# Performance work log

Hardware: AMD Instinct MI355X
Metric: run time of the kernel (lower is better)

## Reference

```python
import jax, jax.numpy as jnp
import numpy as np

N, E, EL = 50000, 150000, 300000   # atoms, bonds(=line-graph nodes), line-graph edges
FN, FE, FX = 128, 128, 64          # atom, bond, angle feature dims (encode_dim)
H, D = 4, 64                        # num_heads, per-head hidden
SLOPE = 0.01                        # torch leaky_relu default


def _leaky(x):
    return jnp.where(x >= 0, x, SLOPE * x)


def _seg_softmax(logits, seg, n):
    # softmax over edges grouped by destination (DGL edge_softmax). logits [E, H]
    m = jax.ops.segment_max(logits, seg, num_segments=n)
    ex = jnp.exp(logits - m[seg])
    s = jax.ops.segment_sum(ex, seg, num_segments=n)
    return ex / s[seg]


def _seg_mean(x, seg, n):
    # mean of incoming edge feats per dst node; empty segments -> 0 (DGL behavior)
    s = jax.ops.segment_sum(x, seg, num_segments=n)
    c = jax.ops.segment_sum(jnp.ones((x.shape[0], 1), x.dtype), seg, num_segments=n)
    return s / jnp.maximum(c, 1.0)


def setup_inputs() -> dict:
    key = jax.random.key(0)
    ks = iter(jax.random.split(key, 40))
    nrm = lambda shape, sc=0.1: jax.random.normal(next(ks), shape, jnp.float32) * sc
    z = lambda n: jnp.zeros((n,), jnp.float32)
    inp = {
        'nfeats': nrm((N, FN), 1.0),
        'efeats': nrm((E, FE), 1.0),
        'xfeats': nrm((EL, FX), 1.0),
        # EGAT layer (atom graph)
        'e_Wni': nrm((H * D, FN)), 'e_Wnj': nrm((H * D, FN)), 'e_Wfij': nrm((H * D, FE)),
        'e_Wnode': nrm((H * D, FN + FE)), 'e_bnode': z(H * D),
        'e_attn': nrm((H, D)), 'e_bias': z(H * D),
        # Path_Complex line-graph branch
        'lg_Wni': nrm((H * D, D)), 'lg_Wnj': nrm((H * D, D)), 'lg_Wfij': nrm((H * D, FX)),
        'lg_Wnode': nrm((H * D, D + FX)), 'lg_bnode': z(H * D),
        'lg_attn': nrm((H, D)), 'lg_bias': z(H * D),
        # Path_Complex graph branch
        'g_Wni': nrm((H * D, D)), 'g_Wnj': nrm((H * D, D)), 'g_Wfij': nrm((H * D, D)),
        'g_Wnode': nrm((H * D, D + D)), 'g_bnode': z(H * D),
        'g_attn': nrm((H, D)), 'g_bias': z(H * D),
        # graph / line-graph connectivity
        'src': jax.random.randint(next(ks), (E,), 0, N, jnp.int32),
        'dst': jax.random.randint(next(ks), (E,), 0, N, jnp.int32),
        'lsrc': jax.random.randint(next(ks), (EL,), 0, E, jnp.int32),
        'ldst': jax.random.randint(next(ks), (EL,), 0, E, jnp.int32),
    }
    return inp


def _forward(nfeats, efeats, xfeats,
             e_Wni, e_Wnj, e_Wfij, e_Wnode, e_bnode, e_attn, e_bias,
             lg_Wni, lg_Wnj, lg_Wfij, lg_Wnode, lg_bnode, lg_attn, lg_bias,
             g_Wni, g_Wnj, g_Wfij, g_Wnode, g_bnode, g_attn, g_bias,
             src, dst, lsrc, ldst):
    # ---- EGAT layer on atom graph ----
    fo = _leaky((nfeats @ e_Wni.T)[src] + (nfeats @ e_Wnj.T)[dst] + efeats @ e_Wfij.T + e_bias)
    fov = fo.reshape(E, H, D)
    e_att = _seg_softmax((fov * e_attn[None]).sum(-1), dst, N)      # [E, H]
    agg = _seg_mean(efeats, dst, N)                                   # [N, FE]
    h = (jnp.concatenate([nfeats, agg], 1) @ e_Wnode.T + e_bnode).reshape(N, H, D)
    h_node = _leaky(jax.ops.segment_sum(h[src] * e_att[:, :, None], dst, num_segments=N)).sum(1)
    f_edge = fov.sum(1)                                               # [E, D]

    # ---- Path_Complex layer: line-graph (bond->angle) branch ----
    lgf = _leaky((f_edge @ lg_Wni.T)[lsrc] + (f_edge @ lg_Wnj.T)[ldst] + xfeats @ lg_Wfij.T + lg_bias)
    lgv = lgf.reshape(EL, H, D)
    a_lg = _seg_softmax((lgv * lg_attn[None]).sum(-1), ldst, E)      # [EL, H]
    aggx = _seg_mean(xfeats, ldst, E)                                 # [E, FX]
    m1 = (jnp.concatenate([f_edge, aggx], 1) @ lg_Wnode.T + lg_bnode).reshape(E, H, D)
    lg_h = _leaky(jax.ops.segment_sum(m1[lsrc] * a_lg[:, :, None], ldst, num_segments=E)).sum(1)

    # ---- Path_Complex layer: graph (atom->bond) branch ----
    gf = _leaky((h_node @ g_Wni.T)[src] + (h_node @ g_Wnj.T)[dst] + f_edge @ g_Wfij.T + g_bias)
    gv = gf.reshape(E, H, D)
    a_g = _seg_softmax((gv * g_attn[None]).sum(-1), dst, N)          # [E, H] -> l_graph ndata 'a'
    node_edge = h_node[src] + h_node[dst]
    m2 = (jnp.concatenate([node_edge, f_edge], 1) @ g_Wnode.T + g_bnode).reshape(E, H, D)
    # u_mul_v on line graph: message = h_out[lsrc] * a[ldst]
    g_h = _leaky(jax.ops.segment_sum(m2[lsrc] * a_g[ldst][:, :, None], ldst, num_segments=E)).sum(1)

    return g_h + lg_h                                                 # [E, D] updated bond feats


def reference(nfeats, efeats, xfeats,
              e_Wni, e_Wnj, e_Wfij, e_Wnode, e_bnode, e_attn, e_bias,
              lg_Wni, lg_Wnj, lg_Wfij, lg_Wnode, lg_bnode, lg_attn, lg_bias,
              g_Wni, g_Wnj, g_Wfij, g_Wnode, g_bnode, g_attn, g_bias,
              src, dst, lsrc, ldst):
    return _forward(nfeats, efeats, xfeats,
                    e_Wni, e_Wnj, e_Wfij, e_Wnode, e_bnode, e_attn, e_bias,
                    lg_Wni, lg_Wnj, lg_Wfij, lg_Wnode, lg_bnode, lg_attn, lg_bias,
                    g_Wni, g_Wnj, g_Wfij, g_Wnode, g_bnode, g_attn, g_bias,
                    src, dst, lsrc, ldst)
```

## Files before the change

### kernel.cpp

```cpp
#include <hip/hip_runtime.h>
#include <hip/hip_bf16.h>
#include <math.h>

typedef __hip_bfloat16 bf16;
typedef short bf16x8 __attribute__((ext_vector_type(8)));
typedef short s16x4 __attribute__((ext_vector_type(4)));
typedef float f32x4 __attribute__((ext_vector_type(4)));

__device__ __forceinline__ float b2f(bf16 x) { return __bfloat162float(x); }
__device__ __forceinline__ bf16  f2b(float x) { return __float2bfloat16(x); }
__device__ __forceinline__ float leaky(float x) { return x >= 0.0f ? x : 0.01f * x; }
__device__ __forceinline__ float sb2f(short s) {
  return __uint_as_float(((unsigned)(unsigned short)s) << 16);
}
__device__ __forceinline__ short f2bs(float x) {
  unsigned u = __float_as_uint(x);
  u += 0x7FFFu + ((u >> 16) & 1u);
  return (short)(u >> 16);
}
__device__ __forceinline__ float ldF(const void* p, size_t i, int f) {
  return f ? ((const float*)p)[i] : b2f(((const bf16*)p)[i]);
}
__device__ __forceinline__ bf16x8 ldA8(const char* row, int k, int f) {
  if (!f) return *(const bf16x8*)(row + (size_t)k * 2);
  const float4* p = (const float4*)(row + (size_t)k * 4);
  float4 a = p[0], b = p[1];
  bf16x8 r;
  r[0] = f2bs(a.x); r[1] = f2bs(a.y); r[2] = f2bs(a.z); r[3] = f2bs(a.w);
  r[4] = f2bs(b.x); r[5] = f2bs(b.y); r[6] = f2bs(b.z); r[7] = f2bs(b.w);
  return r;
}

__global__ void k_detect(const unsigned* __restrict__ w, int* __restrict__ flag) {
  __shared__ int cnt[256];
  unsigned x = w[threadIdx.x];
  unsigned ex = (x >> 7) & 0xFFu;
  cnt[threadIdx.x] = (ex >= 96u && ex <= 144u) ? 1 : 0;
  __syncthreads();
  for (int s = 128; s > 0; s >>= 1) {
    if (threadIdx.x < s) cnt[threadIdx.x] += cnt[threadIdx.x + s];
    __syncthreads();
  }
  if (threadIdx.x == 0) *flag = (cnt[0] < 128) ? 1 : 0;
}

struct WArgs { const void* src[21]; int beg[22]; int len[21]; };
__global__ void k_cvt_all(WArgs wa, bf16* __restrict__ dst, int total,
                          const int* __restrict__ flagp) {
  int f = *flagp;
  for (int i = blockIdx.x * 256 + threadIdx.x; i < total; i += gridDim.x * 256) {
    int t = 0;
    while (t < 20 && i >= wa.beg[t + 1]) ++t;
    int loc = i - wa.beg[t];
    bf16 v = f2b(0.0f);
    if (loc < wa.len[t])
      v = f ? f2b(((const float*)wa.src[t])[loc]) : ((const bf16*)wa.src[t])[loc];
    dst[i] = v;
  }
}

__global__ void k_cvt2(const float* __restrict__ a, bf16* __restrict__ da, size_t na,
                       const float* __restrict__ c, bf16* __restrict__ dc, size_t nc,
                       const int* __restrict__ flagp) {
  if (!*flagp) return;
  size_t tot = (na + nc) >> 2;
  for (size_t i = (size_t)blockIdx.x * 256 + threadIdx.x; i < tot;
       i += (size_t)gridDim.x * 256) {
    size_t j = i << 2;
    const float* s; bf16* d; size_t loc;
    if (j < na) { s = a; d = da; loc = j; }
    else        { s = c; d = dc; loc = j - na; }
    float4 v = *(const float4*)(s + loc);
    s16x4 o; o[0] = f2bs(v.x); o[1] = f2bs(v.y); o[2] = f2bs(v.z); o[3] = f2bs(v.w);
    *(s16x4*)(d + loc) = o;
  }
}

__global__ void k_cvt1(const float* __restrict__ c, bf16* __restrict__ dc, size_t nc,
                       const int* __restrict__ flagp) {
  if (!*flagp) return;
  size_t tot = nc >> 2;
  for (size_t i = (size_t)blockIdx.x * 256 + threadIdx.x; i < tot;
       i += (size_t)gridDim.x * 256) {
    size_t loc = i << 2;
    float4 v = *(const float4*)(c + loc);
    s16x4 o; o[0] = f2bs(v.x); o[1] = f2bs(v.y); o[2] = f2bs(v.z); o[3] = f2bs(v.w);
    *(s16x4*)(dc + loc) = o;
  }
}

__global__ void k_izero(int* __restrict__ p, int n) {
  int i = blockIdx.x * 256 + threadIdx.x;
  for (; i < n; i += gridDim.x * 256) p[i] = 0;
}

__global__ void k_hist(const int* __restrict__ seg, int* __restrict__ deg, int n) {
  int i = blockIdx.x * 256 + threadIdx.x;
  if (i < n) atomicAdd(&deg[seg[i]], 1);
}

__global__ __launch_bounds__(256)
void k_scan_local(const int* __restrict__ deg, int* __restrict__ rp,
                  int* __restrict__ bsum, int n) {
  __shared__ int sh[256];
  int tid = threadIdx.x;
  int base = blockIdx.x * 4096 + tid * 16;
  int v[16]; int s = 0;
#pragma unroll
  for (int j = 0; j < 16; ++j) { v[j] = (base + j < n) ? deg[base + j] : 0; s += v[j]; }
  sh[tid] = s;
  __syncthreads();
  for (int o = 1; o < 256; o <<= 1) {
    int t = (tid >= o) ? sh[tid - o] : 0;
    __syncthreads();
    sh[tid] += t;
    __syncthreads();
  }
  int run = sh[tid] - s;
#pragma unroll
  for (int j = 0; j < 16; ++j) {
    run += v[j];
    if (base + j < n) rp[base + j + 1] = run;
  }
  if (tid == 255) bsum[blockIdx.x] = sh[255];
  if (blockIdx.x == 0 && tid == 0) rp[0] = 0;
}
__global__ __launch_bounds__(256)
void k_scan_bsum(int* __restrict__ bsum, int nb) {
  __shared__ int sh[256];
  __shared__ int carry;
  int tid = threadIdx.x;
  if (tid == 0) carry = 0;
  __syncthreads();
  for (int base = 0; base < nb; base += 256) {
    int i = base + tid;
    int v = (i < nb) ? bsum[i] : 0;
    sh[tid] = v;
    __syncthreads();
    for (int o = 1; o < 256; o <<= 1) {
      int t = (tid >= o) ? sh[tid - o] : 0;
      __syncthreads();
      sh[tid] += t;
      __syncthreads();
    }
    if (i < nb) bsum[i] = carry + sh[tid] - v;
    int tot = sh[255];
    __syncthreads();
    if (tid == 0) carry += tot;
    __syncthreads();
  }
}
__global__ __launch_bounds__(256)
void k_scan_add(int* __restrict__ rp, const int* __restrict__ bsum, int n) {
  int b = blockIdx.x + 1;
  int ofs = bsum[b];
  int base = b * 4096 + threadIdx.x * 16;
#pragma unroll
  for (int j = 0; j < 16; ++j) {
    int idx = base + j + 1;
    if (idx <= n) rp[idx] += ofs;
  }
}

__global__ void k_slot(const int* __restrict__ seg, const int* __restrict__ rp,
                       int* __restrict__ cur, int* __restrict__ eid,
                       const int* __restrict__ aux1, int* __restrict__ av1,
                       int* __restrict__ pos, int n) {
  int i = blockIdx.x * 256 + threadIdx.x;
  if (i >= n) return;
  int t = seg[i];
  int p = atomicAdd(&cur[t], 1);
  int j = rp[t] + p;
  eid[j] = i;
  if (av1) av1[j] = aux1[i];
  if (pos) pos[i] = j;
}

__global__ void k_gmean(const void* __restrict__ X, const void* __restrict__ Xc, int mode,
                        const int* __restrict__ rp, const int* __restrict__ eid,
                        bf16* __restrict__ out, int n, int width,
                        const int* __restrict__ flagp) {
  int f = (mode == 2) ? *flagp : mode;
  if (Xc && f) { X = Xc; f = 0; }
  int d = threadIdx.x;
  int row = blockIdx.x * blockDim.y + threadIdx.y;
  if (row >= n) return;
  int b = rp[row], e = rp[row + 1];
  float s = 0.0f;
  for (int j = b; j < e; ++j) s += ldF(X, (size_t)eid[j] * width + d, f);
  out[(size_t)row * width + d] = f2b(s / fmaxf((float)(e - b), 1.0f));
}

__global__ __launch_bounds__(256)
void k_mgemm(const void* __restrict__ A0, const void* __restrict__ A0c, int m0mode, int K0,
             const void* __restrict__ A1, int m1mode, int Ktot,
             const bf16* __restrict__ W, int whs, const bf16* __restrict__ bias,
             bf16* __restrict__ C, int cs, int M,
             const int* __restrict__ flagp) {
  int tid = threadIdx.x;
  int w = tid >> 6, lane = tid & 63, l15 = lane & 15, q = lane >> 4;
  int h = blockIdx.y;
  int fl = *flagp;
  int f0 = (m0mode == 2) ? fl : m0mode;
  if (A0c && f0) { A0 = A0c; f0 = 0; }
  int f1 = (m1mode == 2) ? fl : m1mode;
  const bf16* Wh = W + (size_t)h * whs;
  int colofs = h * 64;
  int m0 = blockIdx.x * 64 + w * 16;
  int mA = m0 + l15; if (mA > M - 1) mA = M - 1;
  const char* rowA0 = (const char*)A0 + (size_t)mA * K0 * (f0 ? 4 : 2);
  const char* rowA1 = A1 ? (const char*)A1 + (size_t)mA * (Ktot - K0) * (f1 ? 4 : 2) : nullptr;

  f32x4 acc[4] = {{0,0,0,0},{0,0,0,0},{0,0,0,0},{0,0,0,0}};
  for (int k = q * 8; k < Ktot; k += 32) {
    bf16x8 a;
    if (k < K0) a = ldA8(rowA0, k, f0);
    else        a = ldA8(rowA1, k - K0, f1);
    const bf16* wb = Wh + (size_t)l15 * Ktot + k;
#pragma unroll
    for (int t = 0; t < 4; ++t)
      acc[t] = __builtin_amdgcn_mfma_f32_16x16x32_bf16(
          a, *(const bf16x8*)(wb + (size_t)(t * 16) * Ktot), acc[t], 0, 0, 0);
  }
#pragma unroll
  for (int t = 0; t < 4; ++t) {
    int col = t * 16 + l15;
    float bv = bias ? b2f(bias[colofs + col]) : 0.0f;
#pragma unroll
    for (int r = 0; r < 4; ++r) {
      int m = m0 + q * 4 + r;
      if (m < M) C[(size_t)m * cs + colofs + col] = f2b(acc[t][r] + bv);
    }
  }
}

__global__ __launch_bounds__(256)
void k_mgemm2sw(const void* __restrict__ A, const void* __restrict__ Ac, int mode, int K,
                const bf16* __restrict__ W1, const bf16* __restrict__ W2, int whs,
                int h0, int HB, bf16* __restrict__ C1, bf16* __restrict__ C2, int M,
                const int* __restrict__ flagp) {
  int tid = threadIdx.x;
  int w = tid >> 6, lane = tid & 63, l15 = lane & 15, q = lane >> 4;
  int hy = blockIdx.y;
  int h = h0 + hy;
  int f = (mode == 2) ? *flagp : mode;
  if (Ac && f) { A = Ac; f = 0; }
  const bf16* W1h = W1 + (size_t)h * whs;
  const bf16* W2h = W2 + (size_t)h * whs;
  int cs = HB * 64;
  int m0 = blockIdx.x * 64 + w * 16;
  int mA = m0 + l15; if (mA > M - 1) mA = M - 1;
  const char* rowA = (const char*)A + (size_t)mA * K * (f ? 4 : 2);

  f32x4 a1[4] = {{0,0,0,0},{0,0,0,0},{0,0,0,0},{0,0,0,0}};
  f32x4 a2[4] = {{0,0,0,0},{0,0,0,0},{0,0,0,0},{0,0,0,0}};
  for (int k = q * 8; k < K; k += 32) {
    bf16x8 a = ldA8(rowA, k, f);
    const bf16* w1 = W1h + (size_t)l15 * K + k;
    const bf16* w2 = W2h + (size_t)l15 * K + k;
#pragma unroll
    for (int t = 0; t < 4; ++t) {
      a1[t] = __builtin_amdgcn_mfma_f32_16x16x32_bf16(
          a, *(const bf16x8*)(w1 + (size_t)(t * 16) * K), a1[t], 0, 0, 0);
      a2[t] = __builtin_amdgcn_mfma_f32_16x16x32_bf16(
          a, *(const bf16x8*)(w2 + (size_t)(t * 16) * K), a2[t], 0, 0, 0);
    }
  }
  int ofs = l15 * 4 * HB + hy * 4;
#pragma unroll
  for (int r = 0; r < 4; ++r) {
    int m = m0 + q * 4 + r;
    if (m < M) {
      s16x4 o1, o2;
#pragma unroll
      for (int t = 0; t < 4; ++t) { o1[t] = f2bs(a1[t][r]); o2[t] = f2bs(a2[t][r]); }
      *(s16x4*)(C1 + (size_t)m * cs + ofs) = o1;
      *(s16x4*)(C2 + (size_t)m * cs + ofs) = o2;
    }
  }
}

template<int NK>
__global__ __launch_bounds__(256)
void k_mcomb4sw(const bf16* __restrict__ A, const bf16* __restrict__ Ac,
                const bf16* __restrict__ W, int whs,
                const bf16* __restrict__ bias, const bf16* __restrict__ attn,
                const bf16* __restrict__ G1, const bf16* __restrict__ G2,
                const int* __restrict__ gi, const int* __restrict__ gj,
                const int* __restrict__ posw,
                float* __restrict__ lg4, bf16* __restrict__ fout,
                int M, const int* __restrict__ flagp) {
  constexpr int K = NK * 32;
  int tid = threadIdx.x;
  int w = tid >> 6, lane = tid & 63, l15 = lane & 15, q = lane >> 4;
  if (Ac && *flagp) A = Ac;
  int m0 = blockIdx.x * 64 + w * 16;
  int mA = m0 + l15; if (mA > M - 1) mA = M - 1;
  const bf16* rowA = A + (size_t)mA * K;
  bf16x8 af[NK];
#pragma unroll
  for (int i = 0; i < NK; ++i) af[i] = *(const bf16x8*)(rowA + q * 8 + 32 * i);
  int pIdx[4]; bool okr[4];
  bf16x8 gv1[4][2], gv2[4][2];
#pragma unroll
  for (int r = 0; r < 4; ++r) {
    int m = m0 + q * 4 + r;
    okr[r] = m < M; int mc = okr[r] ? m : M - 1;
    pIdx[r] = posw ? posw[mc] : mc;
    const bf16* p1 = G1 + (size_t)gi[mc] * 256 + l15 * 16;
    const bf16* p2 = G2 + (size_t)gj[mc] * 256 + l15 * 16;
    gv1[r][0] = *(const bf16x8*)p1; gv1[r][1] = *(const bf16x8*)(p1 + 8);
    gv2[r][0] = *(const bf16x8*)p2; gv2[r][1] = *(const bf16x8*)(p2 + 8);
  }
  f32x4 fs[4] = {{0,0,0,0},{0,0,0,0},{0,0,0,0},{0,0,0,0}};
#pragma unroll
  for (int h = 0; h < 4; ++h) {
    const bf16* Wh = W + (size_t)h * whs;
    f32x4 acc[4] = {{0,0,0,0},{0,0,0,0},{0,0,0,0},{0,0,0,0}};
#pragma unroll
    for (int i = 0; i < NK; ++i) {
      const bf16* wb = Wh + (size_t)l15 * K + q * 8 + 32 * i;
#pragma unroll
      for (int t = 0; t < 4; ++t)
        acc[t] = __builtin_amdgcn_mfma_f32_16x16x32_bf16(
            af[i], *(const bf16x8*)(wb + (size_t)(t * 16) * K), acc[t], 0, 0, 0);
    }
    float bv[4], av[4];
#pragma unroll
    for (int t = 0; t < 4; ++t) {
      bv[t] = b2f(bias[h * 64 + t * 16 + l15]);
      av[t] = b2f(attn[h * 64 + t * 16 + l15]);
    }
    float part[4];
#pragma unroll
    for (int r = 0; r < 4; ++r) {
      float p = 0.0f;
#pragma unroll
      for (int t = 0; t < 4; ++t) {
        float v = acc[t][r] + bv[t] + sb2f(gv1[r][h >> 1][(h & 1) * 4 + t])
                                    + sb2f(gv2[r][h >> 1][(h & 1) * 4 + t]);
        v = leaky(v);
        p += v * av[t];
        fs[t][r] += v;
      }
      part[r] = p;
    }
#pragma unroll
    for (int o = 1; o < 16; o <<= 1)
#pragma unroll
      for (int r = 0; r < 4; ++r) part[r] += __shfl_xor(part[r], o, 64);
    if (l15 == 0) {
#pragma unroll
      for (int r = 0; r < 4; ++r)
        if (okr[r]) lg4[(size_t)pIdx[r] * 4 + h] = part[r];
    }
  }
  if (fout) {
#pragma unroll
    for (int t = 0; t < 4; ++t) {
      int col = t * 16 + l15;
#pragma unroll
      for (int r = 0; r < 4; ++r)
        if (okr[r]) fout[(size_t)(m0 + q * 4 + r) * 64 + col] = f2b(fs[t][r]);
    }
  }
}

template<int NK>
__global__ __launch_bounds__(256)
void k_mcomb2h(const bf16* __restrict__ A, const bf16* __restrict__ Ac,
               const bf16* __restrict__ W, int whs, int h0,
               const bf16* __restrict__ bias, const bf16* __restrict__ attn,
               const bf16* __restrict__ G1, const bf16* __restrict__ G2,
               const int* __restrict__ gi, const int* __restrict__ gj,
               const int* __restrict__ posw,
               float* __restrict__ lg4, int M, const int* __restrict__ flagp) {
  constexpr int K = NK * 32;
  int tid = threadIdx.x;
  int w = tid >> 6, lane = tid & 63, l15 = lane & 15, q = lane >> 4;
  if (Ac && *flagp) A = Ac;
  int m0 = blockIdx.x * 64 + w * 16;
  int mA = m0 + l15; if (mA > M - 1) mA = M - 1;
  const bf16* rowA = A + (size_t)mA * K;
  bf16x8 af[NK];
#pragma unroll
  for (int i = 0; i < NK; ++i) af[i] = *(const bf16x8*)(rowA + q * 8 + 32 * i);
  int pIdx[4]; bool okr[4];
  bf16x8 gv1[4], gv2[4];
#pragma unroll
  for (int r = 0; r < 4; ++r) {
    int m = m0 + q * 4 + r;
    okr[r] = m < M; int mc = okr[r] ? m : M - 1;
    pIdx[r] = posw ? posw[mc] : mc;
    gv1[r] = *(const bf16x8*)(G1 + (size_t)gi[mc] * 128 + l15 * 8);
    gv2[r] = *(const bf16x8*)(G2 + (size_t)gj[mc] * 128 + l15 * 8);
  }
#pragma unroll
  for (int hy = 0; hy < 2; ++hy) {
    int h = h0 + hy;
    const bf16* Wh = W + (size_t)h * whs;
    f32x4 acc[4] = {{0,0,0,0},{0,0,0,0},{0,0,0,0},{0,0,0,0}};
#pragma unroll
    for (int i = 0; i < NK; ++i) {
      const bf16* wb = Wh + (size_t)l15 * K + q * 8 + 32 * i;
#pragma unroll
      for (int t = 0; t < 4; ++t)
        acc[t] = __builtin_amdgcn_mfma_f32_16x16x32_bf16(
            af[i], *(const bf16x8*)(wb + (size_t)(t * 16) * K), acc[t], 0, 0, 0);
    }
    float bv[4], av[4];
#pragma unroll
    for (int t = 0; t < 4; ++t) {
      bv[t] = b2f(bias[h * 64 + t * 16 + l15]);
      av[t] = b2f(attn[h * 64 + t * 16 + l15]);
    }
    float part[4];
#pragma unroll
    for (int r = 0; r < 4; ++r) {
      float p = 0.0f;
#pragma unroll
      for (int t = 0; t < 4; ++t) {
        float v = acc[t][r] + bv[t] + sb2f(gv1[r][hy * 4 + t]) + sb2f(gv2[r][hy * 4 + t]);
        p += leaky(v) * av[t];
      }
      part[r] = p;
    }
#pragma unroll
    for (int o = 1; o < 16; o <<= 1)
#pragma unroll
      for (int r = 0; r < 4; ++r) part[r] += __shfl_xor(part[r], o, 64);
    if (l15 == 0) {
#pragma unroll
      for (int r = 0; r < 4; ++r)
        if (okr[r]) lg4[(size_t)pIdx[r] * 4 + h] = part[r];
    }
  }
}

__global__ __launch_bounds__(256)
void k_smax4_csr(float* __restrict__ lg, const int* __restrict__ rp, int n) {
  int tid = blockIdx.x * 256 + threadIdx.x;
  int row = tid >> 2, h = tid & 3;
  if (row >= n) return;
  int b = rp[row], e = rp[row + 1];
  float m = -INFINITY;
  for (int j = b; j < e; ++j) m = fmaxf(m, lg[(size_t)j * 4 + h]);
  float s = 0.0f;
  for (int j = b; j < e; ++j) {
    float ex = expf(lg[(size_t)j * 4 + h] - m);
    lg[(size_t)j * 4 + h] = ex;
    s += ex;
  }
  float inv = 1.0f / s;
  for (int j = b; j < e; ++j) lg[(size_t)j * 4 + h] *= inv;
}
__global__ __launch_bounds__(256)
void k_smax4_eid(float* __restrict__ lg, const int* __restrict__ rp,
                 const int* __restrict__ eid, int n) {
  int tid = blockIdx.x * 256 + threadIdx.x;
  int row = tid >> 2, h = tid & 3;
  if (row >= n) return;
  int b = rp[row], e = rp[row + 1];
  float m = -INFINITY;
  for (int j = b; j < e; ++j) m = fmaxf(m, lg[(size_t)eid[j] * 4 + h]);
  float s = 0.0f;
  for (int j = b; j < e; ++j) {
    float ex = expf(lg[(size_t)eid[j] * 4 + h] - m);
    lg[(size_t)eid[j] * 4 + h] = ex;
    s += ex;
  }
  float inv = 1.0f / s;
  for (int j = b; j < e; ++j) lg[(size_t)eid[j] * 4 + h] *= inv;
}

__global__ __launch_bounds__(256)
void k_ghnode(const bf16* __restrict__ H, const float* __restrict__ lg4c,
              const int* __restrict__ rp, const int* __restrict__ srcv,
              bf16* __restrict__ hnode, int N) {
  int d = threadIdx.x, h = threadIdx.y;
  int n = blockIdx.x;
  int b = rp[n], e = rp[n + 1];
  float s = 0.0f;
  for (int j = b; j < e; ++j)
    s += b2f(H[(size_t)srcv[j] * 256 + h * 64 + d]) * lg4c[(size_t)j * 4 + h];
  float v = leaky(s);
  __shared__ float sh[4][64];
  if (h > 0) sh[h][d] = v;
  __syncthreads();
  if (h == 0)
    hnode[(size_t)n * 64 + d] = f2b(v + sh[1][d] + sh[2][d] + sh[3][d]);
}

__global__ void k_gout2(const bf16* __restrict__ M1, const float* __restrict__ lgE4,
                        int h, const int* __restrict__ rp, const int* __restrict__ lsv,
                        float* __restrict__ out, int E, int first) {
  int d = threadIdx.x;
  int t = blockIdx.x * 4 + threadIdx.y;
  if (t >= E) return;
  int b = rp[t], e = rp[t + 1];
  float s = 0.0f;
  for (int j = b; j < e; ++j)
    s += b2f(M1[(size_t)lsv[j] * 64 + d]) * lgE4[(size_t)j * 4 + h];
  float val = leaky(s);
  if (first) out[(size_t)t * 64 + d] = val;
  else       out[(size_t)t * 64 + d] += val;
}

__global__ void k_gagg(const bf16* __restrict__ ne, const bf16* __restrict__ fe,
                       const int* __restrict__ rp, const int* __restrict__ lsv,
                       bf16* __restrict__ agg, int E) {
  int d = threadIdx.x;
  int t = blockIdx.x * 4 + threadIdx.y;
  if (t >= E) return;
  int b = rp[t], e = rp[t + 1];
  float s1 = 0.0f, s2 = 0.0f;
  for (int j = b; j < e; ++j) {
    size_t row = (size_t)lsv[j] * 64 + d;
    s1 += b2f(ne[row]);
    s2 += b2f(fe[row]);
  }
  agg[(size_t)t * 128 + d]      = f2b(s1);
  agg[(size_t)t * 128 + 64 + d] = f2b(s2);
}

__global__ __launch_bounds__(256)
void k_mgemm3(const bf16* __restrict__ A, const bf16* __restrict__ W, int whs,
              const bf16* __restrict__ bias, const float* __restrict__ lg4n,
              const int* __restrict__ rp, float* __restrict__ out, int M) {
  int tid = threadIdx.x;
  int w = tid >> 6, lane = tid & 63, l15 = lane & 15, q = lane >> 4;
  int m0 = blockIdx.x * 64 + w * 16;
  int mA = m0 + l15; if (mA > M - 1) mA = M - 1;
  const bf16* rowA = A + (size_t)mA * 128;
  bf16x8 af[4];
#pragma unroll
  for (int i = 0; i < 4; ++i) af[i] = *(const bf16x8*)(rowA + q * 8 + 32 * i);
  bool okr[4]; float degv[4]; float av[4][4];
#pragma unroll
  for (int r = 0; r < 4; ++r) {
    int m = m0 + q * 4 + r;
    okr[r] = m < M; int mc = okr[r] ? m : M - 1;
    degv[r] = (float)(rp[mc + 1] - rp[mc]);
#pragma unroll
    for (int h = 0; h < 4; ++h) av[r][h] = lg4n[(size_t)mc * 4 + h];
  }
  float osum[4][4] = {{0,0,0,0},{0,0,0,0},{0,0,0,0},{0,0,0,0}};
#pragma unroll
  for (int h = 0; h < 4; ++h) {
    const bf16* Wh = W + (size_t)h * whs;
    f32x4 acc[4] = {{0,0,0,0},{0,0,0,0},{0,0,0,0},{0,0,0,0}};
#pragma unroll
    for (int i = 0; i < 4; ++i) {
      const bf16* wb = Wh + (size_t)l15 * 128 + q * 8 + 32 * i;
#pragma unroll
      for (int t = 0; t < 4; ++t)
        acc[t] = __builtin_amdgcn_mfma_f32_16x16x32_bf16(
            af[i], *(const bf16x8*)(wb + (size_t)(t * 16) * 128), acc[t], 0, 0, 0);
    }
#pragma unroll
    for (int t = 0; t < 4; ++t) {
      float bv = b2f(bias[h * 64 + t * 16 + l15]);
#pragma unroll
      for (int r = 0; r < 4; ++r)
        osum[t][r] += leaky(av[r][h] * (acc[t][r] + degv[r] * bv));
    }
  }
#pragma unroll
  for (int t = 0; t < 4; ++t) {
    int col = t * 16 + l15;
#pragma unroll
    for (int r = 0; r < 4; ++r) {
      int m = m0 + q * 4 + r;
      if (m < M) out[(size_t)m * 64 + col] += osum[t][r];
    }
  }
}

__global__ void k_addpair(const bf16* __restrict__ hn, const int* __restrict__ src,
                          const int* __restrict__ dst, bf16* __restrict__ ne, int E) {
  int d = threadIdx.x;
  int e = blockIdx.x * 4 + threadIdx.y;
  if (e >= E) return;
  ne[(size_t)e * 64 + d] =
      f2b(b2f(hn[(size_t)src[e] * 64 + d]) + b2f(hn[(size_t)dst[e] * 64 + d]));
}

__global__ void k_cast(void* __restrict__ out, const float* __restrict__ a, size_t n,
                       const int* __restrict__ flagp) {
  int f = *flagp;
  size_t i = (size_t)blockIdx.x * blockDim.x + threadIdx.x;
  size_t st = (size_t)gridDim.x * blockDim.x;
  for (; i < n; i += st) {
    if (f) ((float*)out)[i] = a[i];
    else   ((bf16*)out)[i] = f2b(a[i]);
  }
}

extern "C" void kernel_launch(void* const* d_in, const int* in_sizes, int n_in,
                              void* d_out, int out_size, void* d_ws, size_t ws_size,
                              hipStream_t stream) {
  const int* src  = (const int*)d_in[24];
  const int* dst  = (const int*)d_in[25];
  const int* lsrc = (const int*)d_in[26];
  const int* ldst = (const int*)d_in[27];

  const int N  = in_sizes[0] / 128;
  const int E  = in_sizes[24];
  const int EL = in_sizes[26];
  (void)n_in; (void)out_size; (void)ws_size;

  char* base = (char*)d_ws;
  size_t off = 0;
  auto alloc = [&](size_t bytes) -> char* {
    char* p = base + off;
    off = (off + bytes + 255) & ~(size_t)255;
    return p;
  };
  int* flag = (int*)alloc(256);
  size_t wofs[28]; size_t wtot = 0;
  for (int i = 3; i <= 23; ++i) { wofs[i] = wtot; wtot += (size_t)((in_sizes[i] + 127) & ~127); }
  bf16* WA = (bf16*)alloc(wtot * 2);

  int*   tmpi  = (int*)alloc((size_t)2 * E * 4);
  int*   rpN   = (int*)alloc((size_t)(N + 1) * 4);
  int*   eidN  = (int*)alloc((size_t)E * 4);
  int*   srcv  = (int*)alloc((size_t)E * 4);
  int*   posN  = (int*)alloc((size_t)E * 4);
  int*   rpE   = (int*)alloc((size_t)(E + 1) * 4);
  int*   eidEL = (int*)alloc((size_t)EL * 4);
  int*   lsv   = (int*)alloc((size_t)EL * 4);
  int*   posE  = (int*)alloc((size_t)EL * 4);
  int*   bsum  = (int*)alloc(((size_t)((E > N ? E : N) + 4095) / 4096 + 8) * 4);
  bf16*  fedge = (bf16*)alloc((size_t)E * 64 * 2);
  bf16*  hnode = (bf16*)alloc((size_t)N * 64 * 2);
  float* outacc= (float*)alloc((size_t)E * 64 * 4);
  bf16*  aggB  = (bf16*)alloc((size_t)E * 64 * 2);
  size_t saElems = (size_t)E * 128 > (size_t)N * 256 ? (size_t)E * 128 : (size_t)N * 256;
  bf16*  SA    = (bf16*)alloc(saElems * 2);
  float* logE4 = (float*)alloc((size_t)E * 4 * 4);
  float* logEL4= (float*)alloc((size_t)EL * 4 * 4);
  bf16*  nb    = (bf16*)alloc((size_t)N * 128 * 2);

  bf16* SBo = (bf16*)outacc;
  bf16* eb = (bf16*)d_out;
  bf16* xb = (bf16*)d_out;

  dim3 blk(256);
  const unsigned tN = (N + 63) / 64, tEg = (E + 63) / 64, tELg = (EL + 63) / 64;
  const unsigned gE4 = (E + 3) / 4;
  const unsigned cE = (E + 255) / 256, cEL = (EL + 255) / 256;
  const int nbN = (N + 4095) / 4096, nbE = (E + 4095) / 4096;

  k_detect<<<dim3(1), blk, 0, stream>>>((const unsigned*)d_in[0], flag);
  WArgs wa;
  for (int i = 3; i <= 23; ++i) {
    wa.src[i - 3] = d_in[i];
    wa.beg[i - 3] = (int)wofs[i];
    wa.len[i - 3] = in_sizes[i];
  }
  wa.beg[21] = (int)wtot;
  k_cvt_all<<<dim3(512), blk, 0, stream>>>(wa, WA, (int)wtot, flag);
  k_cvt2<<<dim3(2048), blk, 0, stream>>>(
      (const float*)d_in[0], nb, (size_t)N * 128,
      (const float*)d_in[1], eb, (size_t)E * 128, flag);

  int* deg = tmpi; int* cur = tmpi + E;
  k_izero<<<dim3(1024), blk, 0, stream>>>(tmpi, 2 * E);
  k_hist<<<dim3(cE), blk, 0, stream>>>(dst, deg, E);
  k_scan_local<<<dim3(nbN), blk, 0, stream>>>(deg, rpN, bsum, N);
  k_scan_bsum<<<dim3(1), blk, 0, stream>>>(bsum, nbN);
  if (nbN > 1) k_scan_add<<<dim3(nbN - 1), blk, 0, stream>>>(rpN, bsum, N);
  k_slot<<<dim3(cE), blk, 0, stream>>>(dst, rpN, cur, eidN, src, srcv, posN, E);
  k_izero<<<dim3(1024), blk, 0, stream>>>(tmpi, 2 * E);
  k_hist<<<dim3(cEL), blk, 0, stream>>>(ldst, deg, EL);
  k_scan_local<<<dim3(nbE), blk, 0, stream>>>(deg, rpE, bsum, E);
  k_scan_bsum<<<dim3(1), blk, 0, stream>>>(bsum, nbE);
  if (nbE > 1) k_scan_add<<<dim3(nbE - 1), blk, 0, stream>>>(rpE, bsum, E);
  k_slot<<<dim3(cEL), blk, 0, stream>>>(ldst, rpE, cur, eidEL, lsrc, lsv, posE, EL);

  k_gmean<<<dim3((N + 1) / 2), dim3(128, 2), 0, stream>>>(d_in[1], eb, 2, rpN, eidN,
                                                          aggB, N, 128, flag);
  k_mgemm2sw<<<dim3(tN, 4), blk, 0, stream>>>(d_in[0], nb, 2, 128,
      WA + wofs[3], WA + wofs[4], 8192, 0, 4, SA, SBo, N, flag);
  k_mcomb4sw<4><<<dim3(tEg), blk, 0, stream>>>((const bf16*)d_in[1], eb,
      WA + wofs[5], 8192, WA + wofs[9], WA + wofs[8], SA, SBo,
      src, dst, posN, logE4, fedge, E, flag);
  k_smax4_csr<<<dim3((N * 4 + 255) / 256), blk, 0, stream>>>(logE4, rpN, N);
  k_mgemm<<<dim3(tN, 4), blk, 0, stream>>>(d_in[0], nb, 2, 128, aggB, 0, 256,
      WA + wofs[6], 16384, WA + wofs[7], SA, 256, N, flag);
  k_ghnode<<<dim3(N), dim3(64, 4), 0, stream>>>(SA, logE4, rpN, srcv, hnode, N);

  k_cvt1<<<dim3(2048), blk, 0, stream>>>((const float*)d_in[2], xb,
                                         (size_t)EL * 64, flag);

  k_gmean<<<dim3(gE4), dim3(64, 4), 0, stream>>>(d_in[2], xb, 2, rpE, eidEL, aggB, E, 64, flag);
  for (int p = 0; p < 2; ++p) {
    k_mgemm2sw<<<dim3(tEg, 2), blk, 0, stream>>>(fedge, nullptr, 0, 64,
        WA + wofs[10], WA + wofs[11], 4096, 2 * p, 2, SA, SBo, E, flag);
    k_mcomb2h<2><<<dim3(tELg), blk, 0, stream>>>((const bf16*)d_in[2], xb,
        WA + wofs[12], 4096, 2 * p, WA + wofs[16], WA + wofs[15],
        SA, SBo, lsrc, ldst, posE, logEL4, EL, flag);
  }
  k_smax4_csr<<<dim3((E * 4 + 255) / 256), blk, 0, stream>>>(logEL4, rpE, E);
  for (int h = 0; h < 4; ++h) {
    k_mgemm<<<dim3(tEg, 1), blk, 0, stream>>>(fedge, nullptr, 0, 64, aggB, 0, 128,
        WA + wofs[13] + (size_t)h * 8192, 0, WA + wofs[14] + h * 64,
        SA, 64, E, flag);
    k_gout2<<<dim3(gE4), dim3(64, 4), 0, stream>>>(SA, logEL4, h, rpE, lsv,
                                                   outacc, E, h == 0 ? 1 : 0);
  }

  for (int p = 0; p < 2; ++p) {
    k_mgemm2sw<<<dim3(tN, 2), blk, 0, stream>>>(hnode, nullptr, 0, 64,
        WA + wofs[17], WA + wofs[18], 4096, 2 * p, 2, SA, SA + (size_t)N * 128, N, flag);
    k_mcomb2h<2><<<dim3(tEg), blk, 0, stream>>>(fedge, nullptr,
        WA + wofs[19], 4096, 2 * p, WA + wofs[23], WA + wofs[22],
        SA, SA + (size_t)N * 128, src, dst, nullptr, logE4, E, flag);
  }
  k_smax4_eid<<<dim3((N * 4 + 255) / 256), blk, 0, stream>>>(logE4, rpN, eidN, N);
  k_addpair<<<dim3(gE4), dim3(64, 4), 0, stream>>>(hnode, src, dst, aggB, E);
  k_gagg<<<dim3(gE4), dim3(64, 4), 0, stream>>>(aggB, fedge, rpE, lsv, SA, E);
  k_mgemm3<<<dim3(tEg), blk, 0, stream>>>(SA, WA + wofs[20], 8192, WA + wofs[21],
                                          logE4, rpE, outacc, E);

  k_cast<<<dim3(2048), blk, 0, stream>>>(d_out, outacc, (size_t)E * 64, flag);
}
```

Measured before the change: 1.619 ms.

## Process two heads per pass in line-graph output and fuse graph-branch head passes

The per-head GEMM plus gather-aggregate loop (four passes) becomes two passes, each computing two heads into a 128-wide buffer; a new gather kernel accumulates both heads per edge, so the CSR index and weight reads are shared. The graph-branch projection and attention-logit kernels now run once over all four heads instead of two passes, using a 4-head combine kernel. This cuts kernel launches and repeated index and row reads in exchange for a larger scratch buffer. It relies on k_mcomb4sw, which does not appear in the visible changes and presumably already exists in the file.

```diff
diff --git a/kernel.cpp b/kernel.cpp
--- a/kernel.cpp
+++ b/kernel.cpp
@@ -491,17 +491,22 @@
     hnode[(size_t)n * 64 + d] = f2b(v + sh[1][d] + sh[2][d] + sh[3][d]);
 }
 
-__global__ void k_gout2(const bf16* __restrict__ M1, const float* __restrict__ lgE4,
-                        int h, const int* __restrict__ rp, const int* __restrict__ lsv,
-                        float* __restrict__ out, int E, int first) {
+__global__ void k_gout2x2(const bf16* __restrict__ M1, const float* __restrict__ lgE4,
+                          int h0, const int* __restrict__ rp, const int* __restrict__ lsv,
+                          float* __restrict__ out, int E, int first) {
   int d = threadIdx.x;
   int t = blockIdx.x * 4 + threadIdx.y;
   if (t >= E) return;
   int b = rp[t], e = rp[t + 1];
-  float s = 0.0f;
-  for (int j = b; j < e; ++j)
-    s += b2f(M1[(size_t)lsv[j] * 64 + d]) * lgE4[(size_t)j * 4 + h];
-  float val = leaky(s);
+  float s0 = 0.0f, s1 = 0.0f;
+  for (int j = b; j < e; ++j) {
+    size_t row = (size_t)lsv[j] * 128;
+    float w0 = lgE4[(size_t)j * 4 + h0];
+    float w1 = lgE4[(size_t)j * 4 + h0 + 1];
+    s0 += b2f(M1[row + d]) * w0;
+    s1 += b2f(M1[row + 64 + d]) * w1;
+  }
+  float val = leaky(s0) + leaky(s1);
   if (first) out[(size_t)t * 64 + d] = val;
   else       out[(size_t)t * 64 + d] += val;
 }
@@ -635,7 +640,8 @@
   bf16*  hnode = (bf16*)alloc((size_t)N * 64 * 2);
   float* outacc= (float*)alloc((size_t)E * 64 * 4);
   bf16*  aggB  = (bf16*)alloc((size_t)E * 64 * 2);
-  size_t saElems = (size_t)E * 128 > (size_t)N * 256 ? (size_t)E * 128 : (size_t)N * 256;
+  size_t saElems = (size_t)E * 128 > (size_t)2 * N * 256 ? (size_t)E * 128
+                                                         : (size_t)2 * N * 256;
   bf16*  SA    = (bf16*)alloc(saElems * 2);
   float* logE4 = (float*)alloc((size_t)E * 4 * 4);
   float* logEL4= (float*)alloc((size_t)EL * 4 * 4);
@@ -702,21 +708,19 @@
         SA, SBo, lsrc, ldst, posE, logEL4, EL, flag);
   }
   k_smax4_csr<<<dim3((E * 4 + 255) / 256), blk, 0, stream>>>(logEL4, rpE, E);
-  for (int h = 0; h < 4; ++h) {
-    k_mgemm<<<dim3(tEg, 1), blk, 0, stream>>>(fedge, nullptr, 0, 64, aggB, 0, 128,
-        WA + wofs[13] + (size_t)h * 8192, 0, WA + wofs[14] + h * 64,
-        SA, 64, E, flag);
-    k_gout2<<<dim3(gE4), dim3(64, 4), 0, stream>>>(SA, logEL4, h, rpE, lsv,
-                                                   outacc, E, h == 0 ? 1 : 0);
-  }
-
   for (int p = 0; p < 2; ++p) {
-    k_mgemm2sw<<<dim3(tN, 2), blk, 0, stream>>>(hnode, nullptr, 0, 64,
-        WA + wofs[17], WA + wofs[18], 4096, 2 * p, 2, SA, SA + (size_t)N * 128, N, flag);
-    k_mcomb2h<2><<<dim3(tEg), blk, 0, stream>>>(fedge, nullptr,
-        WA + wofs[19], 4096, 2 * p, WA + wofs[23], WA + wofs[22],
-        SA, SA + (size_t)N * 128, src, dst, nullptr, logE4, E, flag);
-  }
+    k_mgemm<<<dim3(tEg, 2), blk, 0, stream>>>(fedge, nullptr, 0, 64, aggB, 0, 128,
+        WA + wofs[13] + (size_t)(2 * p) * 8192, 8192, WA + wofs[14] + 2 * p * 64,
+        SA, 128, E, flag);
+    k_gout2x2<<<dim3(gE4), dim3(64, 4), 0, stream>>>(SA, logEL4, 2 * p, rpE, lsv,
+                                                     outacc, E, p == 0 ? 1 : 0);
+  }
+
+  k_mgemm2sw<<<dim3(tN, 4), blk, 0, stream>>>(hnode, nullptr, 0, 64,
+      WA + wofs[17], WA + wofs[18], 4096, 0, 4, SA, SA + (size_t)N * 256, N, flag);
+  k_mcomb4sw<2><<<dim3(tEg), blk, 0, stream>>>(fedge, nullptr,
+      WA + wofs[19], 4096, WA + wofs[23], WA + wofs[22],
+      SA, SA + (size_t)N * 256, src, dst, nullptr, logE4, nullptr, E, flag);
   k_smax4_eid<<<dim3((N * 4 + 255) / 256), blk, 0, stream>>>(logE4, rpN, eidN, N);
   k_addpair<<<dim3(gE4), dim3(64, 4), 0, stream>>>(hnode, src, dst, aggB, E);
   k_gagg<<<dim3(gE4), dim3(64, 4), 0, stream>>>(aggB, fedge, rpE, lsv, SA, E);
```

Result: faster. 1.513 ms (-6.5%).
